# Kernel optimization log

Hardware: AMD Instinct MI355X
Metric: run time of the kernel (lower is better)

Reference implementation:

```python
import jax, jax.numpy as jnp
import numpy as np

ITE = 20
LAM = 0.1
MU1_0 = 0.1
MU2_0 = 0.1
RHO = 1.05


def _shrink(x, t):
    # soft-threshold: sign(x) * max(|x| - t, 0)
    return jnp.sign(x) * jnp.maximum(jnp.abs(x) - t, 0.0)


# circular forward differences (kernel [1, -1]) along W, H, and spectral (C) axes
def _diff_h(x):
    return x - jnp.roll(x, -1, axis=-1)

def _diff_v(x):
    return x - jnp.roll(x, -1, axis=-2)

def _diff_s(x):
    return x - jnp.roll(x, -1, axis=1)

# adjoint (transpose) differences used inside the FFT-based TV solve
def _diff_hT(x):
    return x - jnp.roll(x, 1, axis=-1)

def _diff_vT(x):
    return x - jnp.roll(x, 1, axis=-2)

def _diff_sT(x):
    return x - jnp.roll(x, 1, axis=1)


def _demo(C, H, W):
    # |F(Dh)|^2 + |F(Dv)|^2 + |F(Ds)|^2 for circular [1,-1] kernels:
    # |1 - exp(-2*pi*i*k/L)|^2 = 2 - 2*cos(2*pi*k/L) along each axis.
    dc = 2.0 - 2.0 * jnp.cos(2.0 * jnp.pi * jnp.arange(C) / C)
    dh = 2.0 - 2.0 * jnp.cos(2.0 * jnp.pi * jnp.arange(H) / H)
    dw = 2.0 - 2.0 * jnp.cos(2.0 * jnp.pi * jnp.arange(W) / W)
    return (dc[:, None, None] + dh[None, :, None] + dw[None, None, :]).astype(jnp.float32)  # [C,H,W]


def _hwtv3d(Y, inW):
    N, C, H, W = Y.shape
    demo = _demo(C, H, W)  # [C,H,W], broadcasts over batch
    mu1, mu2, lam = MU1_0, MU2_0, LAM
    zero = jnp.float32(0.0)
    G1 = G21 = G22 = G23 = zero  # scalar zeros, broadcast like the torch `0`
    Z = Y
    X = Y
    DhZ, DvZ, DsZ = _diff_h(Z), _diff_v(Z), _diff_s(Z)
    for _ in range(ITE):
        Uh = _shrink(DhZ - G21 / mu2, lam / mu2)
        Uv = _shrink(DvZ - G22 / mu2, lam / mu2)
        Us = _shrink(DsZ - G23 / mu2, lam / mu2)
        # TV_solver3D: (mu1*I + mu2*(Dh^T Dh + Dv^T Dv + Ds^T Ds))^{-1} applied via 3D FFT
        numer = mu1 * (X + G1 / mu1) + mu2 * (
            _diff_hT(Uh + G21 / mu2) + _diff_vT(Uv + G22 / mu2) + _diff_sT(Us + G23 / mu2)
        )
        F = jnp.fft.fftn(numer, axes=(1, 2, 3))
        Z = jnp.real(jnp.fft.ifftn(F / (mu1 + mu2 * demo), axes=(1, 2, 3)))
        DhZ, DvZ, DsZ = _diff_h(Z), _diff_v(Z), _diff_s(Z)
        X = (inW * Y + mu1 * Z - G1) / (inW + mu1)
        G1 = G1 + mu1 * (X - Z)
        G21 = G21 + mu2 * (Uh - DhZ)
        G22 = G22 + mu2 * (Uv - DvZ)
        G23 = G23 + mu2 * (Us - DsZ)
        mu1 = RHO * mu1
        mu2 = RHO * mu2
    return Z


def setup_inputs() -> dict:
    key = jax.random.key(0)
    k1, k2 = jax.random.split(key)
    Y = jax.random.normal(k1, (4, 31, 128, 128), dtype=jnp.float32)
    inW = jax.random.uniform(k2, (4, 31, 128, 128), dtype=jnp.float32)
    return {"Y": Y, "inW": inW}


def reference(Y, inW):
    return _hwtv3d(Y, inW)
```

## Files before the change

kernel.cpp:

```cpp
#include <hip/hip_runtime.h>
#include <hip/hip_fp16.h>
#include <math.h>

#define N_ 4
#define C_ 31
#define H_ 128
#define W_ 128
#define TOTAL (N_*C_*H_*W_)
#define CV_ (C_*H_*W_)
#define PI_F 3.14159265358979f
#define RHO_F 1.05f
#define INV_RHO (1.0f/1.05f)
#define NORM2 (1.0f/16384.0f)

typedef __attribute__((ext_vector_type(2))) float v2f;
typedef __attribute__((ext_vector_type(2))) _Float16 h2f;

__device__ __forceinline__ v2f cmulv(v2f a, v2f b){
  v2f t = a.x * b;
  v2f s = (v2f){-a.y, a.y};
  return t + s * b.yx;
}
__device__ __forceinline__ v2f shflv(v2f v, int m){
  v2f r; r.x = __shfl_xor(v.x, m, 64); r.y = __shfl_xor(v.y, m, 64); return r;
}
__device__ __forceinline__ h2f shflh(h2f v, int m){
  float f = __builtin_bit_cast(float, v);
  f = __shfl_xor(f, m, 64);
  return __builtin_bit_cast(h2f, f);
}
__device__ __forceinline__ float shrinkf(float x, float t){
  return copysignf(fmaxf(fabsf(x) - t, 0.0f), x);
}
__device__ __forceinline__ uint packh2(v2f v){
  union{__half2 h2; uint u;} cv; cv.h2 = __floats2half2_rn(v.x, v.y); return cv.u;
}
__device__ __forceinline__ v2f unpackh2(uint u){
  union{uint uu; __half2 h2;} cv; cv.uu = u;
  float2 f = __half22float2(cv.h2);
  return (v2f){f.x, f.y};
}
__device__ __forceinline__ v2f h2v(__half2 h){
  float2 f = __half22float2(h);
  return (v2f){f.x, f.y};
}
__device__ __forceinline__ v2f vupd(v2f D, v2f vo, float thr){
  const float aa = 1.0f + INV_RHO;
  return (v2f){
    shrinkf(aa*D.x - vo.x*INV_RHO, thr) + (vo.x - D.x)*INV_RHO,
    shrinkf(aa*D.y - vo.y*INV_RHO, thr) + (vo.y - D.y)*INV_RHO};
}
__device__ __forceinline__ void load_tw(const v2f* __restrict__ lut, v2f* tw, int lane){
  #pragma unroll
  for (int i = 0; i < 7; ++i) tw[i] = lut[i*64 + lane];
}

__device__ __forceinline__ void fft128_fwd(v2f& a, v2f& b, const v2f* twf, int t){
  v2f u = a + b;
  v2f v = cmulv(a - b, twf[0]);
  #pragma unroll
  for (int i = 1; i < 7; ++i){
    int sp = 64 >> i;
    bool up = (t & sp) != 0;
    v2f pu = shflv(u, sp);
    v2f du = up ? pu - u : u + pu;
    u = cmulv(du, twf[i]);
    v2f pv = shflv(v, sp);
    v2f dv = up ? pv - v : v + pv;
    v = cmulv(dv, twf[i]);
  }
  a = u; b = v;
}

__device__ __forceinline__ void fft128_inv(v2f& a, v2f& b, const v2f* twi, int t){
  v2f u = a, v = b;
  #pragma unroll
  for (int i = 6; i >= 1; --i){
    int sp = 64 >> i;
    bool up = (t & sp) != 0;
    v2f pu = shflv(u, sp);
    v2f e  = up ? pu : u;
    v2f o  = up ? u  : pu;
    v2f wo = cmulv(o, twi[i]);
    u = up ? e - wo : e + wo;
    v2f pv = shflv(v, sp);
    v2f ev = up ? pv : v;
    v2f ov = up ? v  : pv;
    v2f wv = cmulv(ov, twi[i]);
    v = up ? ev - wv : ev + wv;
  }
  v2f tv = cmulv(v, twi[0]);
  a = u + tv;
  b = u - tv;
}

__device__ __forceinline__ void fft128_inv_h2(h2f& are, h2f& aim, h2f& bre, h2f& bim,
    const uint* __restrict__ twc, const uint* __restrict__ tws, int t){
  #pragma unroll
  for (int i = 6; i >= 1; --i){
    int sp = 64 >> i;
    bool up = (t & sp) != 0;
    h2f c2 = __builtin_bit_cast(h2f, twc[i*64 + t]);
    h2f s2 = __builtin_bit_cast(h2f, tws[i*64 + t]);
    h2f pre = shflh(are, sp), pim = shflh(aim, sp);
    h2f e_re = up ? pre : are, e_im = up ? pim : aim;
    h2f o_re = up ? are : pre, o_im = up ? aim : pim;
    are = e_re + (o_re*c2 - o_im*s2);
    aim = e_im + (o_re*s2 + o_im*c2);
    pre = shflh(bre, sp); pim = shflh(bim, sp);
    e_re = up ? pre : bre; e_im = up ? pim : bim;
    o_re = up ? bre : pre; o_im = up ? bim : pim;
    bre = e_re + (o_re*c2 - o_im*s2);
    bim = e_im + (o_re*s2 + o_im*c2);
  }
  h2f c0 = __builtin_bit_cast(h2f, twc[t]);
  h2f s0 = __builtin_bit_cast(h2f, tws[t]);
  h2f tr = bre*c0 - bim*s0;
  h2f ti = bre*s0 + bim*c0;
  h2f ur = are, ui = aim;
  are = ur + tr; aim = ui + ti;
  bre = ur - tr; bim = ui - ti;
}

__device__ __forceinline__ void fft128_fwd_h2(h2f& are, h2f& aim, h2f& bre, h2f& bim,
    const uint* __restrict__ twc, const uint* __restrict__ tws, int t){
  h2f c0 = __builtin_bit_cast(h2f, twc[t]);
  h2f s0 = __builtin_bit_cast(h2f, tws[t]);
  h2f dre = are - bre, dim = aim - bim;
  h2f ure = are + bre, uim = aim + bim;
  h2f vre = dre*c0 - dim*s0;
  h2f vim = dre*s0 + dim*c0;
  #pragma unroll
  for (int i = 1; i < 7; ++i){
    int sp = 64 >> i;
    bool up = (t & sp) != 0;
    h2f c2 = __builtin_bit_cast(h2f, twc[i*64 + t]);
    h2f s2 = __builtin_bit_cast(h2f, tws[i*64 + t]);
    h2f sg = up ? (h2f){(_Float16)-1.0f, (_Float16)-1.0f} : (h2f){(_Float16)1.0f, (_Float16)1.0f};
    h2f pre = shflh(ure, sp), pim = shflh(uim, sp);
    h2f d1 = sg*ure + pre, d2 = sg*uim + pim;
    ure = d1*c2 - d2*s2; uim = d1*s2 + d2*c2;
    pre = shflh(vre, sp); pim = shflh(vim, sp);
    d1 = sg*vre + pre; d2 = sg*vim + pim;
    vre = d1*c2 - d2*s2; vim = d1*s2 + d2*c2;
  }
  are = ure; aim = uim; bre = vre; bim = vim;
}

__global__ __launch_bounds__(128) void kern_init(v2f* __restrict__ twf_lut,
    v2f* __restrict__ twi_lut, float* __restrict__ dtab,
    uint* __restrict__ twihc, uint* __restrict__ twihs,
    uint* __restrict__ twfhc, uint* __restrict__ twfhs)
{
  int t = threadIdx.x;
  if (t < 64){
    float s, c;
    sincosf(-2.0f*PI_F*(float)t/128.0f, &s, &c);
    twf_lut[t] = (v2f){c, s};
    { union{__half2 h; uint u;} cc, ss;
      cc.h = __floats2half2_rn(c, c); ss.h = __floats2half2_rn(s, s);
      twfhc[t] = cc.u; twfhs[t] = ss.u; }
    sincosf(+2.0f*PI_F*(float)t/128.0f, &s, &c);
    twi_lut[t] = (v2f){c, s};
    { union{__half2 h; uint u;} cc, ss;
      cc.h = __floats2half2_rn(c, c); ss.h = __floats2half2_rn(s, s);
      twihc[t] = cc.u; twihs[t] = ss.u; }
    #pragma unroll
    for (int i = 1; i < 7; ++i){
      int sp = 64 >> i;
      float angf = (t & sp) ? -2.0f*PI_F*(float)(t&(sp-1))/(float)(2*sp) : 0.0f;
      sincosf(angf, &s, &c);
      twf_lut[i*64 + t] = (v2f){c, s};
      { union{__half2 h; uint u;} cc, ss;
        cc.h = __floats2half2_rn(c, c); ss.h = __floats2half2_rn(s, s);
        twfhc[i*64 + t] = cc.u; twfhs[i*64 + t] = ss.u; }
      float angi = +2.0f*PI_F*(float)(t&(sp-1))/(float)(2*sp);
      sincosf(angi, &s, &c);
      twi_lut[i*64 + t] = (v2f){c, s};
      float ch = c, sh = s;
      if (t & sp){ ch = -ch; sh = -sh; }
      union{__half2 h; uint u;} cc, ss;
      cc.h = __floats2half2_rn(ch, ch); ss.h = __floats2half2_rn(sh, sh);
      twihc[i*64 + t] = cc.u; twihs[i*64 + t] = ss.u;
    }
  }
  dtab[t] = 2.0f - 2.0f*cosf(2.0f*PI_F*(float)t/128.0f);
}

__global__ __launch_bounds__(256) void kern_pack(const float* __restrict__ Y,
    const float* __restrict__ W, uint2* __restrict__ YWp)
{
  int i = blockIdx.x * 256 + threadIdx.x;
  int pair = i / CV_, j = i - pair*CV_;
  long b0 = (long)(2*pair)*CV_ + j, b1 = b0 + CV_;
  union{__half2 h2; uint u;} a, b;
  a.h2 = __floats2half2_rn(Y[b0], W[b0]);
  b.h2 = __floats2half2_rn(Y[b1], W[b1]);
  YWp[i] = make_uint2(a.u, b.u);
}

__global__ __launch_bounds__(256) void kern_fwd0(const float* __restrict__ Y,
    __half2* __restrict__ Vho, __half2* __restrict__ Vvo, __half2* __restrict__ Vso,
    __half2* __restrict__ A, float thr, const v2f* __restrict__ twf_lut)
{
  __shared__ v2f  zbuf[26][128];
  __shared__ uint zs[25][128];
  int tid = threadIdx.x, lane = tid & 63, wv = tid >> 6;
  int b = blockIdx.x;
  int ht = b & 15, c = (b >> 4) % C_, pair = b / (16*C_);
  int h0 = ht * 8;
  int cm1 = c ? c-1 : C_-1, cp1 = (c == C_-1) ? 0 : c+1;
  long v0 = (long)(2*pair)*CV_, v1 = v0 + CV_;

  for (int u = wv; u < 26; u += 4){
    int cc, h;
    if (u < 10){ cc = c; h = (h0 - 1 + u) & (H_-1); }
    else if (u < 18){ cc = cm1; h = h0 + u - 10; }
    else { cc = cp1; h = h0 + u - 18; }
    long rb = ((long)cc*H_ + h)*W_;
    #pragma unroll
    for (int e = 0; e < 2; ++e){
      int w = lane + 64*e;
      zbuf[u][w] = (v2f){Y[v0+rb+w], Y[v1+rb+w]};
    }
  }
  __syncthreads();

  v2f q[2][2], vs[2][2], vsm[2][2];
  #pragma unroll
  for (int r = 0; r < 2; ++r){
    int i = wv + 4*r, h = h0 + i;
    long pv = ((long)(pair*C_ + c)*H_ + h)*W_;
    #pragma unroll
    for (int e = 0; e < 2; ++e){
      int w = lane + 64*e;
      v2f z0 = zbuf[i+1][w];
      v2f zw = zbuf[i+1][(w+1)&(W_-1)];
      v2f zh = zbuf[i+2][w];
      v2f zc = zbuf[18+i][w];
      v2f zm = zbuf[10+i][w];
      v2f vh = (v2f){shrinkf(z0.x-zw.x,thr), shrinkf(z0.y-zw.y,thr)};
      v2f vv = (v2f){shrinkf(z0.x-zh.x,thr), shrinkf(z0.y-zh.y,thr)};
      v2f vsl= (v2f){shrinkf(z0.x-zc.x,thr), shrinkf(z0.y-zc.y,thr)};
      vsm[r][e] = (v2f){shrinkf(zm.x-z0.x,thr), shrinkf(zm.y-z0.y,thr)};
      Vho[pv+w] = __floats2half2_rn(vh.x, vh.y);
      Vvo[pv+w] = __floats2half2_rn(vv.x, vv.y);
      Vso[pv+w] = __floats2half2_rn(vsl.x, vsl.y);
      zs[i][w]   = packh2(vh);
      zs[9+i][w] = packh2(vv);
      vs[r][e] = vsl;
      q[r][e]  = z0;
    }
  }
  if (wv == 0){
    #pragma unroll
    for (int e = 0; e < 2; ++e){
      int w = lane + 64*e;
      v2f z0 = zbuf[0][w], zh = zbuf[1][w];
      v2f vvm = (v2f){shrinkf(z0.x-zh.x,thr), shrinkf(z0.y-zh.y,thr)};
      zs[8][w] = packh2(vvm);
    }
  }
  __syncthreads();

  v2f twf[7]; load_tw(twf_lut, twf, lane);
  #pragma unroll
  for (int r = 0; r < 2; ++r){
    int i = wv + 4*r;
    v2f nm[2];
    #pragma unroll
    for (int e = 0; e < 2; ++e){
      int w = lane + 64*e;
      v2f vh  = unpackh2(zs[i][w]);
      v2f vhm = unpackh2(zs[i][(w+W_-1)&(W_-1)]);
      v2f vv  = unpackh2(zs[9+i][w]);
      v2f vvm = unpackh2(zs[8+i][w]);
      nm[e] = q[r][e] + (vh - vhm) + (vv - vvm) + (vs[r][e] - vsm[r][e]);
    }
    fft128_fwd(nm[0], nm[1], twf, lane);
    zs[17+i][lane]    = packh2(nm[0]);
    zs[17+i][lane+64] = packh2(nm[1]);
  }
  __syncthreads();
  int4* A4 = (int4*)A;
  int p = tid >> 1, hq = tid & 1;
  union{int4 v; uint e[4];} u;
  #pragma unroll
  for (int j = 0; j < 4; ++j) u.e[j] = zs[17 + 4*hq + j][p];
  A4[((long)(pair*W_ + p)*C_ + c)*32 + 2*ht + hq] = u.v;
}

__global__ __launch_bounds__(1024) void kern_CH(__half2* __restrict__ A,
    const uint* __restrict__ twfhc, const uint* __restrict__ twfhs,
    const uint* __restrict__ twihc, const uint* __restrict__ twihs,
    const float* __restrict__ dtab)
{
  __shared__ v2f slab[C_][H_];
  __shared__ v2f slab2[C_][H_];
  int tid = threadIdx.x, lane = tid & 63, wv = tid >> 6;
  int bid = blockIdx.x;
  int w = bid & (W_-1);
  const int4* g4 = (const int4*)(A + (long)bid * C_ * H_);

  if (tid < 992){
    union { int4 v; __half2 e[4]; } u;
    u.v = g4[tid];
    int c = tid >> 5, hb = (tid & 31) << 2;
    #pragma unroll
    for (int j = 0; j < 4; ++j) slab[c][hb+j] = h2v(u.e[j]);
  }
  __syncthreads();

  {
    int c1 = wv, c2 = (wv + 16 < C_) ? wv + 16 : (C_-1);
    v2f a0 = slab[c1][lane], b0 = slab[c1][lane+64];
    v2f a1 = slab[c2][lane], b1 = slab[c2][lane+64];
    h2f are = (h2f){(_Float16)a0.x, (_Float16)a1.x};
    h2f aim = (h2f){(_Float16)a0.y, (_Float16)a1.y};
    h2f bre = (h2f){(_Float16)b0.x, (_Float16)b1.x};
    h2f bim = (h2f){(_Float16)b0.y, (_Float16)b1.y};
    fft128_fwd_h2(are, aim, bre, bim, twfhc, twfhs, lane);
    slab[c1][lane]    = (v2f){(float)are.x, (float)aim.x};
    slab[c1][lane+64] = (v2f){(float)bre.x, (float)bim.x};
    if (wv + 16 < C_){
      slab[c2][lane]    = (v2f){(float)are.y, (float)aim.y};
      slab[c2][lane+64] = (v2f){(float)bre.y, (float)bim.y};
    }
  }
  __syncthreads();

  {
    int col = tid & (H_-1), cb = tid >> 7, c0 = cb * 4;
    int fh = __brev(col) >> 25;
    int fw = __brev(w)   >> 25;
    float beta = 1.0f + dtab[fh] + dtab[fw];
    float a2 = beta + 2.0f;
    float s  = sqrtf(a2*a2 - 4.0f);
    float rg = (a2 - s) * 0.5f;
    float gt[9];
    gt[0] = NORM2 / s;
    #pragma unroll
    for (int t = 1; t < 9; ++t) gt[t] = gt[t-1] * rg;

    v2f win[20];
    #pragma unroll
    for (int i = 0; i < 20; ++i){
      int ci = c0 - 8 + i;
      if (ci < 0) ci += C_;
      if (ci >= C_) ci -= C_;
      win[i] = slab[ci][col];
    }
    #pragma unroll
    for (int j = 0; j < 4; ++j){
      v2f o = (v2f){0.0f, 0.0f};
      #pragma unroll
      for (int t = -8; t <= 8; ++t){
        float gv = gt[t < 0 ? -t : t];
        o += gv * win[j + 8 - t];
      }
      int c = c0 + j;
      if (c < C_) slab2[c][col] = o;
    }
  }
  __syncthreads();

  {
    int c1 = wv, c2 = (wv + 16 < C_) ? wv + 16 : (C_-1);
    v2f a0 = slab2[c1][lane], b0 = slab2[c1][lane+64];
    v2f a1 = slab2[c2][lane], b1 = slab2[c2][lane+64];
    h2f are = (h2f){(_Float16)a0.x, (_Float16)a1.x};
    h2f aim = (h2f){(_Float16)a0.y, (_Float16)a1.y};
    h2f bre = (h2f){(_Float16)b0.x, (_Float16)b1.x};
    h2f bim = (h2f){(_Float16)b0.y, (_Float16)b1.y};
    fft128_inv_h2(are, aim, bre, bim, twihc, twihs, lane);
    slab2[c1][lane]    = (v2f){(float)are.x, (float)aim.x};
    slab2[c1][lane+64] = (v2f){(float)bre.x, (float)bim.x};
    if (wv + 16 < C_){
      slab2[c2][lane]    = (v2f){(float)are.y, (float)aim.y};
      slab2[c2][lane+64] = (v2f){(float)bre.y, (float)bim.y};
    }
  }
  __syncthreads();
  int4* go4 = (int4*)(A + (long)bid * C_ * H_);
  if (tid < 992){
    int c = tid >> 5, hb = (tid & 31) << 2;
    union { int4 v; __half2 e[4]; } u;
    #pragma unroll
    for (int j = 0; j < 4; ++j){
      v2f f = slab2[c][hb+j];
      u.e[j] = __floats2half2_rn(f.x, f.y);
    }
    go4[tid] = u.v;
  }
}

__global__ __launch_bounds__(1024) void kern_CA(
    const __half2* __restrict__ Ain, __half2* __restrict__ Aout,
    const __half2* __restrict__ Vhi, const __half2* __restrict__ Vvi, const __half2* __restrict__ Vsi,
    __half2* __restrict__ Vho, __half2* __restrict__ Vvo, __half2* __restrict__ Vso,
    const uint2* __restrict__ YWp, __half2* __restrict__ G1,
    float mu, float thrn, float invmun, int firstG,
    const uint* __restrict__ twfhc, const uint* __restrict__ twfhs,
    const uint* __restrict__ twihc, const uint* __restrict__ twihs)
{
  __shared__ v2f  zbuf[56][128];
  __shared__ uint zs[80][128];
  int tid = threadIdx.x, lane = tid & 63, wv = tid >> 6;
  int b = blockIdx.x;
  int ht = b & 15, ct = (b >> 4) & 7, pair = b >> 7;
  int c0 = 4*ct, nc = (ct == 7) ? 3 : 4;
  int h0 = ht * 8;
  int k = wv >> 3, hl = wv & 7;
  int cm1 = c0 ? c0-1 : C_-1;
  int cp4 = (c0 + 4) % C_;

  int cA = c0 + 2*k;
  int cB = (c0 + 2*k + 1) % C_;
  int cAm1 = cA ? cA-1 : C_-1;
  int h = h0 + hl;
  long pvA = ((long)(pair*C_ + cA)*H_ + h)*W_;
  long pvB = ((long)(pair*C_ + cB)*H_ + h)*W_;
  long pvM = ((long)(pair*C_ + cAm1)*H_ + h)*W_;
  uint pf_vh[2][2], pf_vv[2][2], pf_vs[2][2], pf_vsmA[2], pf_g1[2][2], pf_vvh[2];
  uint2 pf_yw[2][2];
  #pragma unroll
  for (int e = 0; e < 2; ++e){
    int w = lane + 64*e;
    pf_vh[0][e] = *(const uint*)(Vhi + pvA + w);
    pf_vh[1][e] = *(const uint*)(Vhi + pvB + w);
    pf_vv[0][e] = *(const uint*)(Vvi + pvA + w);
    pf_vv[1][e] = *(const uint*)(Vvi + pvB + w);
    pf_vs[0][e] = *(const uint*)(Vsi + pvA + w);
    pf_vs[1][e] = *(const uint*)(Vsi + pvB + w);
    pf_vsmA[e]  = *(const uint*)(Vsi + pvM + w);
    pf_yw[0][e] = YWp[pvA + w];
    pf_yw[1][e] = YWp[pvB + w];
    pf_g1[0][e] = *(const uint*)(G1 + pvA + w);
    pf_g1[1][e] = *(const uint*)(G1 + pvB + w);
  }
  if (wv < 4){
    int cc = (c0 + wv) % C_;
    long pvh = ((long)(pair*C_ + cc)*H_ + ((h0+H_-1)&(H_-1)))*W_;
    #pragma unroll
    for (int e = 0; e < 2; ++e){
      int w = lane + 64*e;
      pf_vvh[e] = *(const uint*)(Vvi + pvh + w);
    }
  }

  const int4* A4 = (const int4*)Ain;
  #pragma unroll
  for (int kk = 0; kk < 3; ++kk){
    int s = tid + 1024*kk;
    if (s < 2560){
      int qq = s >> 7, w = s & 127;
      int cc, hq, base;
      if (qq < 16){
        cc = (c0 + (qq >> 2)) % C_;
        hq = (2*ht - 1 + (qq & 3)) & 31;
        base = (qq >> 2)*16 + (qq & 3)*4;
      } else if (qq < 18){
        cc = cm1; hq = 2*ht + (qq - 16); base = 64 + (qq - 16)*4;
      } else {
        cc = cp4; hq = 2*ht + (qq - 18); base = 72 + (qq - 18)*4;
      }
      union{int4 v; uint e[4];} u;
      u.v = A4[((long)(pair*W_ + w)*C_ + cc)*32 + hq];
      #pragma unroll
      for (int j = 0; j < 4; ++j) zs[base+j][w] = u.e[j];
    }
  }
  __syncthreads();

  {
    #pragma unroll
    for (int kk = 0; kk < 2; ++kk){
      int j = wv + 16*kk;
      if (kk == 1 && j >= 28) break;
      int bP = 2*j, bQ = 2*j + 1;
      int zrP = (bP < 40) ? ((bP/10)*16 + (bP%10) + 3) : (bP + 24);
      int zrQ = (bQ < 40) ? ((bQ/10)*16 + (bQ%10) + 3) : (bQ + 24);
      uint r0a = zs[zrP][lane],    r1a = zs[zrQ][lane];
      uint r0b = zs[zrP][lane+64], r1b = zs[zrQ][lane+64];
      h2f are = __builtin_bit_cast(h2f, (r0a & 0xffffu) | (r1a << 16));
      h2f aim = __builtin_bit_cast(h2f, (r0a >> 16) | (r1a & 0xffff0000u));
      h2f bre = __builtin_bit_cast(h2f, (r0b & 0xffffu) | (r1b << 16));
      h2f bim = __builtin_bit_cast(h2f, (r0b >> 16) | (r1b & 0xffff0000u));
      fft128_inv_h2(are, aim, bre, bim, twihc, twihs, lane);
      zbuf[bP][lane]    = (v2f){(float)are.x, (float)aim.x};
      zbuf[bP][lane+64] = (v2f){(float)bre.x, (float)bim.x};
      zbuf[bQ][lane]    = (v2f){(float)are.y, (float)aim.y};
      zbuf[bQ][lane+64] = (v2f){(float)bre.y, (float)bim.y};
    }
  }
  __syncthreads();

  v2f q2[2][2], vs2[2][2], vsm2[2][2];
  #pragma unroll
  for (int s = 0; s < 2; ++s){
    int cL = 2*k + s;
    bool valid = (cL < nc);
    int zb0 = 10*cL + 1 + hl;
    int zbc = (cL < 3) ? (10*(cL+1) + 1 + hl) : (48 + hl);
    int zbm = (cL == 0) ? (40 + hl) : (10*(cL-1) + 1 + hl);
    long pv = (s == 0) ? pvA : pvB;
    #pragma unroll
    for (int e = 0; e < 2; ++e){
      int w = lane + 64*e;
      v2f z0 = zbuf[zb0][w];
      v2f zw = zbuf[zb0][(w+1)&(W_-1)];
      v2f zh = zbuf[zb0+1][w];
      v2f zc = zbuf[zbc][w];
      v2f vh  = vupd(z0 - zw, unpackh2(pf_vh[s][e]), thrn);
      v2f vv  = vupd(z0 - zh, unpackh2(pf_vv[s][e]), thrn);
      v2f vsl = vupd(z0 - zc, unpackh2(pf_vs[s][e]), thrn);
      if (s == 0){
        v2f zm = zbuf[zbm][w];
        vsm2[0][e] = vupd(zm - z0, unpackh2(pf_vsmA[e]), thrn);
        vsm2[1][e] = vsl;
      }
      if (valid){
        Vho[pv+w] = __floats2half2_rn(vh.x, vh.y);
        Vvo[pv+w] = __floats2half2_rn(vv.x, vv.y);
        Vso[pv+w] = __floats2half2_rn(vsl.x, vsl.y);
      }
      zs[cL*8 + hl][w]      = packh2(vh);
      zs[32 + cL*8 + hl][w] = packh2(vv);
      vs2[s][e] = vsl;
      v2f a0 = unpackh2(pf_yw[s][e].x);
      v2f a1 = unpackh2(pf_yw[s][e].y);
      v2f g1 = firstG ? (v2f){0.0f, 0.0f} : unpackh2(pf_g1[s][e]);
      float x0 = (a0.y*a0.x + mu*z0.x - g1.x) * __builtin_amdgcn_rcpf(a0.y + mu);
      float x1 = (a1.y*a1.x + mu*z0.y - g1.y) * __builtin_amdgcn_rcpf(a1.y + mu);
      float g10 = g1.x + mu*(x0 - z0.x);
      float g11 = g1.y + mu*(x1 - z0.y);
      if (valid) G1[pv+w] = __floats2half2_rn(g10, g11);
      q2[s][e] = (v2f){x0 + g10*invmun, x1 + g11*invmun};
    }
  }
  if (wv < 4){
    int zb = 10*wv;
    #pragma unroll
    for (int e = 0; e < 2; ++e){
      int w = lane + 64*e;
      v2f z0 = zbuf[zb][w], zh = zbuf[zb+1][w];
      v2f vvm = vupd(z0 - zh, unpackh2(pf_vvh[e]), thrn);
      zs[64 + wv][w] = packh2(vvm);
    }
  }
  __syncthreads();

  {
    v2f nm[2][2];
    #pragma unroll
    for (int s = 0; s < 2; ++s){
      int cL = 2*k + s;
      #pragma unroll
      for (int e = 0; e < 2; ++e){
        int w = lane + 64*e;
        v2f vh  = unpackh2(zs[cL*8 + hl][w]);
        v2f vhm = unpackh2(zs[cL*8 + hl][(w+W_-1)&(W_-1)]);
        v2f vv  = unpackh2(zs[32 + cL*8 + hl][w]);
        v2f vvm = (hl == 0) ? unpackh2(zs[64 + cL][w]) : unpackh2(zs[32 + cL*8 + hl - 1][w]);
        nm[s][e] = q2[s][e] + (vh - vhm) + (vv - vvm) + (vs2[s][e] - vsm2[s][e]);
      }
    }
    bool validB = (2*k + 1 < nc);
    if (!validB){ nm[1][0] = nm[0][0]; nm[1][1] = nm[0][1]; }
    h2f are = (h2f){(_Float16)nm[0][0].x, (_Float16)nm[1][0].x};
    h2f aim = (h2f){(_Float16)nm[0][0].y, (_Float16)nm[1][0].y};
    h2f bre = (h2f){(_Float16)nm[0][1].x, (_Float16)nm[1][1].x};
    h2f bim = (h2f){(_Float16)nm[0][1].y, (_Float16)nm[1][1].y};
    fft128_fwd_h2(are, aim, bre, bim, twfhc, twfhs, lane);
    uint a_ = __builtin_bit_cast(uint, are), ai_ = __builtin_bit_cast(uint, aim);
    uint b_ = __builtin_bit_cast(uint, bre), bi_ = __builtin_bit_cast(uint, bim);
    uint* tb = (uint*)zbuf;
    int r0 = (2*k)*8 + hl, r1 = (2*k+1)*8 + hl;
    tb[r0*128 + lane]      = (a_ & 0xffffu) | (ai_ << 16);
    tb[r0*128 + lane + 64] = (b_ & 0xffffu) | (bi_ << 16);
    if (validB){
      tb[r1*128 + lane]      = (a_ >> 16) | (ai_ & 0xffff0000u);
      tb[r1*128 + lane + 64] = (b_ >> 16) | (bi_ & 0xffff0000u);
    }
  }
  __syncthreads();

  {
    int q = tid >> 7, w = tid & 127;
    int cL = q >> 1, hq2 = q & 1;
    if (cL < nc){
      const uint* tb = (const uint*)zbuf;
      int4* Ao4 = (int4*)Aout;
      union{int4 v; uint e[4];} uo;
      #pragma unroll
      for (int j = 0; j < 4; ++j) uo.e[j] = tb[(cL*8 + 4*hq2 + j)*128 + w];
      Ao4[((long)(pair*W_ + w)*C_ + (c0+cL))*32 + 2*ht + hq2] = uo.v;
    }
  }
}

__global__ __launch_bounds__(256) void kern_last(const __half2* __restrict__ A,
    float* __restrict__ Z, const v2f* __restrict__ twi_lut)
{
  __shared__ uint zs[8][128];
  int tid = threadIdx.x, lane = tid & 63, wv = tid >> 6;
  int b = blockIdx.x;
  int ht = b & 15, c = (b >> 4) % C_, pair = b / (16*C_);
  int h0 = ht * 8;
  const int4* A4 = (const int4*)A;
  {
    int p = tid >> 1, hq = tid & 1;
    union{int4 v; uint e[4];} u;
    u.v = A4[((long)(pair*W_ + p)*C_ + c)*32 + 2*ht + hq];
    #pragma unroll
    for (int j = 0; j < 4; ++j) zs[4*hq + j][p] = u.e[j];
  }
  __syncthreads();
  v2f twi[7]; load_tw(twi_lut, twi, lane);
  long v0 = (long)(2*pair)*CV_, v1 = v0 + CV_;
  #pragma unroll
  for (int r = 0; r < 2; ++r){
    int i = wv + 4*r, h = h0 + i;
    v2f a = unpackh2(zs[i][lane]);
    v2f bb = unpackh2(zs[i][lane+64]);
    fft128_inv(a, bb, twi, lane);
    long rb = ((long)c*H_ + h)*W_;
    Z[v0+rb+lane]    = a.x;  Z[v1+rb+lane]    = a.y;
    Z[v0+rb+lane+64] = bb.x; Z[v1+rb+lane+64] = bb.y;
  }
}

extern "C" void kernel_launch(void* const* d_in, const int* in_sizes, int n_in,
                              void* d_out, int out_size, void* d_ws, size_t ws_size,
                              hipStream_t stream)
{
  const float* Y   = (const float*)d_in[0];
  const float* inW = (const float*)d_in[1];
  float* Z = (float*)d_out;

  v2f*   twf_lut = (v2f*)d_ws;
  v2f*   twi_lut = twf_lut + 7*64;
  float* dtab    = (float*)(twi_lut + 7*64);
  uint*  twihc   = (uint*)(dtab + 128);
  uint*  twihs   = twihc + 7*64;
  uint*  twfhc   = twihs + 7*64;
  uint*  twfhs   = twfhc + 7*64;
  char*  fields  = (char*)d_ws + 16384;

  const int HT = TOTAL/2;
  uint2*   YWp = (uint2*)fields;
  __half2* G1  = (__half2*)(YWp + HT);
  __half2* Vh0 = G1  + HT;
  __half2* Vv0 = Vh0 + HT;
  __half2* Vs0 = Vv0 + HT;
  __half2* Vh1 = Vs0 + HT;
  __half2* Vv1 = Vh1 + HT;
  __half2* Vs1 = Vv1 + HT;
  __half2* A0  = Vs1 + HT;
  __half2* A1  = A0  + HT;
  __half2* Vh[2] = {Vh0, Vh1};
  __half2* Vv[2] = {Vv0, Vv1};
  __half2* Vs[2] = {Vs0, Vs1};
  __half2* Ab[2] = {A0, A1};

  kern_init<<<dim3(1), dim3(128), 0, stream>>>(twf_lut, twi_lut, dtab, twihc, twihs, twfhc, twfhs);
  kern_pack<<<dim3(2*CV_/256), dim3(256), 0, stream>>>(Y, inW, YWp);
  kern_fwd0<<<dim3(2*C_*16), dim3(256), 0, stream>>>(Y, Vh0, Vv0, Vs0, A0, 1.0f, twf_lut);

  float mu = 0.1f;
  for (int t = 0; t < 19; ++t){
    kern_CH<<<dim3(2*W_), dim3(1024), 0, stream>>>(Ab[t&1], twfhc, twfhs, twihc, twihs, dtab);
    float mun = mu * RHO_F;
    kern_CA<<<dim3(256), dim3(1024), 0, stream>>>(
        Ab[t&1], Ab[(t+1)&1],
        Vh[t&1], Vv[t&1], Vs[t&1],
        Vh[(t+1)&1], Vv[(t+1)&1], Vs[(t+1)&1],
        YWp, G1, mu, 0.1f/mun, 1.0f/mun, (t==0) ? 1 : 0,
        twfhc, twfhs, twihc, twihs);
    mu = mun;
  }
  kern_CH<<<dim3(2*W_), dim3(1024), 0, stream>>>(Ab[1], twfhc, twfhs, twihc, twihs, dtab);
  kern_last<<<dim3(2*C_*16), dim3(256), 0, stream>>>(Ab[1], Z, twi_lut);
}
```

Baseline: 523.6 us.

## Fuse iteration loop into one cooperative persistent kernel with grid syncs

Replaces the 39 separate kern_CH/kern_CA launches with a single cooperative kernel of 256 blocks that loops over iterations and separates the phases with grid.sync(). Shared memory is carved from one 96KB static buffer that both phase bodies share. The aim is to remove per-launch overhead and inter-kernel gaps. In exchange it requires all 256 blocks of 1024 threads to be co-resident, and grid-wide barriers can cost more than kernel boundaries.

```diff
diff --git a/kernel.cpp b/kernel.cpp
--- a/kernel.cpp
+++ b/kernel.cpp
@@ -1,4 +1,5 @@
 #include <hip/hip_runtime.h>
+#include <hip/hip_cooperative_groups.h>
 #include <hip/hip_fp16.h>
 #include <math.h>
 
@@ -290,13 +291,13 @@
   A4[((long)(pair*W_ + p)*C_ + c)*32 + 2*ht + hq] = u.v;
 }
 
-__global__ __launch_bounds__(1024) void kern_CH(__half2* __restrict__ A,
+__device__ __forceinline__ void ch_body(__half2* __restrict__ A, char* smem,
     const uint* __restrict__ twfhc, const uint* __restrict__ twfhs,
     const uint* __restrict__ twihc, const uint* __restrict__ twihs,
     const float* __restrict__ dtab)
 {
-  __shared__ v2f slab[C_][H_];
-  __shared__ v2f slab2[C_][H_];
+  v2f (*slab)[H_]  = (v2f(*)[H_])(smem);
+  v2f (*slab2)[H_] = (v2f(*)[H_])(smem + 31744);
   int tid = threadIdx.x, lane = tid & 63, wv = tid >> 6;
   int bid = blockIdx.x;
   int w = bid & (W_-1);
@@ -394,17 +395,17 @@
   }
 }
 
-__global__ __launch_bounds__(1024) void kern_CA(
+__device__ __forceinline__ void ca_body(
     const __half2* __restrict__ Ain, __half2* __restrict__ Aout,
     const __half2* __restrict__ Vhi, const __half2* __restrict__ Vvi, const __half2* __restrict__ Vsi,
     __half2* __restrict__ Vho, __half2* __restrict__ Vvo, __half2* __restrict__ Vso,
     const uint2* __restrict__ YWp, __half2* __restrict__ G1,
-    float mu, float thrn, float invmun, int firstG,
+    float mu, float thrn, float invmun, int firstG, char* smem,
     const uint* __restrict__ twfhc, const uint* __restrict__ twfhs,
     const uint* __restrict__ twihc, const uint* __restrict__ twihs)
 {
-  __shared__ v2f  zbuf[56][128];
-  __shared__ uint zs[80][128];
+  v2f  (*zbuf)[128] = (v2f(*)[128])(smem);
+  uint (*zs)[128]   = (uint(*)[128])(smem + 57344);
   int tid = threadIdx.x, lane = tid & 63, wv = tid >> 6;
   int b = blockIdx.x;
   int ht = b & 15, ct = (b >> 4) & 7, pair = b >> 7;
@@ -599,6 +600,40 @@
   }
 }
 
+__global__ __launch_bounds__(1024) void kern_loop(
+    __half2* A0, __half2* A1,
+    __half2* Vh0, __half2* Vv0, __half2* Vs0,
+    __half2* Vh1, __half2* Vv1, __half2* Vs1,
+    const uint2* YWp, __half2* G1,
+    const uint* twfhc, const uint* twfhs,
+    const uint* twihc, const uint* twihs,
+    const float* dtab)
+{
+  __shared__ __align__(16) char smem[98304];
+  cooperative_groups::grid_group grid = cooperative_groups::this_grid();
+  float mu = 0.1f;
+  #pragma unroll 1
+  for (int t = 0; t < 19; ++t){
+    __half2* Acur = (t & 1) ? A1 : A0;
+    __half2* Anxt = (t & 1) ? A0 : A1;
+    __half2* Vhc  = (t & 1) ? Vh1 : Vh0;
+    __half2* Vvc  = (t & 1) ? Vv1 : Vv0;
+    __half2* Vsc  = (t & 1) ? Vs1 : Vs0;
+    __half2* Vhn  = (t & 1) ? Vh0 : Vh1;
+    __half2* Vvn  = (t & 1) ? Vv0 : Vv1;
+    __half2* Vsn  = (t & 1) ? Vs0 : Vs1;
+    ch_body(Acur, smem, twfhc, twfhs, twihc, twihs, dtab);
+    grid.sync();
+    float mun = mu * RHO_F;
+    ca_body(Acur, Anxt, Vhc, Vvc, Vsc, Vhn, Vvn, Vsn, YWp, G1,
+            mu, 0.1f/mun, 1.0f/mun, (t == 0) ? 1 : 0, smem,
+            twfhc, twfhs, twihc, twihs);
+    mu = mun;
+    grid.sync();
+  }
+  ch_body(A1, smem, twfhc, twfhs, twihc, twihs, dtab);
+}
+
 __global__ __launch_bounds__(256) void kern_last(const __half2* __restrict__ A,
     float* __restrict__ Z, const v2f* __restrict__ twi_lut)
 {
@@ -658,27 +693,23 @@
   __half2* Vs1 = Vv1 + HT;
   __half2* A0  = Vs1 + HT;
   __half2* A1  = A0  + HT;
-  __half2* Vh[2] = {Vh0, Vh1};
-  __half2* Vv[2] = {Vv0, Vv1};
-  __half2* Vs[2] = {Vs0, Vs1};
-  __half2* Ab[2] = {A0, A1};
 
   kern_init<<<dim3(1), dim3(128), 0, stream>>>(twf_lut, twi_lut, dtab, twihc, twihs, twfhc, twfhs);
   kern_pack<<<dim3(2*CV_/256), dim3(256), 0, stream>>>(Y, inW, YWp);
   kern_fwd0<<<dim3(2*C_*16), dim3(256), 0, stream>>>(Y, Vh0, Vv0, Vs0, A0, 1.0f, twf_lut);
 
-  float mu = 0.1f;
-  for (int t = 0; t < 19; ++t){
-    kern_CH<<<dim3(2*W_), dim3(1024), 0, stream>>>(Ab[t&1], twfhc, twfhs, twihc, twihs, dtab);
-    float mun = mu * RHO_F;
-    kern_CA<<<dim3(256), dim3(1024), 0, stream>>>(
-        Ab[t&1], Ab[(t+1)&1],
-        Vh[t&1], Vv[t&1], Vs[t&1],
-        Vh[(t+1)&1], Vv[(t+1)&1], Vs[(t+1)&1],
-        YWp, G1, mu, 0.1f/mun, 1.0f/mun, (t==0) ? 1 : 0,
-        twfhc, twfhs, twihc, twihs);
-    mu = mun;
-  }
-  kern_CH<<<dim3(2*W_), dim3(1024), 0, stream>>>(Ab[1], twfhc, twfhs, twihc, twihs, dtab);
-  kern_last<<<dim3(2*C_*16), dim3(256), 0, stream>>>(Ab[1], Z, twi_lut);
-}
+  {
+    void* kargs[] = {
+      (void*)&A0, (void*)&A1,
+      (void*)&Vh0, (void*)&Vv0, (void*)&Vs0,
+      (void*)&Vh1, (void*)&Vv1, (void*)&Vs1,
+      (void*)&YWp, (void*)&G1,
+      (void*)&twfhc, (void*)&twfhs, (void*)&twihc, (void*)&twihs,
+      (void*)&dtab
+    };
+    hipLaunchCooperativeKernel((const void*)kern_loop, dim3(256), dim3(1024),
+                               kargs, 0, stream);
+  }
+
+  kern_last<<<dim3(2*C_*16), dim3(256), 0, stream>>>(A1, Z, twi_lut);
+}
```

Measured after the change: 1.891 ms. +261.1%, slower.
